# Performance work log

Measured on AMD Instinct MI355X. Metric: run time of the kernel, lower is better.

Reference implementation:

```python
import jax, jax.numpy as jnp
import numpy as np

N = 10000
E = 160000
EPS = 1e-5


def _bn(x, g, b):
    # BatchNorm1d over node dim, training-mode batch stats, biased variance
    m = jnp.mean(x, axis=0)
    v = jnp.mean((x - m) ** 2, axis=0)
    return (x - m) * jax.lax.rsqrt(v + EPS) * g + b


def _graph_conv(x, src, dst, ew, w_rel, b_rel, w_root):
    # PyG GraphConv: lin_rel(scatter_add(ew * x[src] -> dst)) + lin_root(x)
    agg = jax.ops.segment_sum(x[src] * ew[:, None], dst, num_segments=N)
    return agg @ w_rel + b_rel + x @ w_root


def setup_inputs() -> dict:
    key = jax.random.key(0)
    ks = jax.random.split(key, 16)
    x = jax.random.normal(ks[0], (N, 517), jnp.float32)
    edge_index = jax.random.randint(ks[1], (2, E), 0, N, dtype=jnp.int64)
    edge_weight = jax.random.uniform(ks[2], (E,), jnp.float32)

    def lin(k, fi, fo):
        return jax.random.normal(k, (fi, fo), jnp.float32) / np.sqrt(fi)

    d = dict(x=x, edge_index=edge_index, edge_weight=edge_weight)
    dims = [(517, 256), (256, 128), (128, 64)]
    for i, (fi, fo) in enumerate(dims, 1):
        d[f"w_rel{i}"] = lin(ks[3 * i], fi, fo)
        d[f"b_rel{i}"] = jnp.zeros((fo,), jnp.float32)
        d[f"w_root{i}"] = lin(ks[3 * i + 1], fi, fo)
        d[f"bn{i}_g"] = jnp.ones((fo,), jnp.float32)
        d[f"bn{i}_b"] = jnp.zeros((fo,), jnp.float32)
    d["w_lin"] = lin(ks[13], 64, 1)
    d["b_lin"] = jnp.zeros((1,), jnp.float32)
    return d


def reference(x, edge_index, edge_weight,
              w_rel1, b_rel1, w_root1, bn1_g, bn1_b,
              w_rel2, b_rel2, w_root2, bn2_g, bn2_b,
              w_rel3, b_rel3, w_root3, bn3_g, bn3_b,
              w_lin, b_lin):
    src, dst = edge_index[0], edge_index[1]
    h = jax.nn.relu(_bn(_graph_conv(x, src, dst, edge_weight, w_rel1, b_rel1, w_root1), bn1_g, bn1_b))
    h = jax.nn.relu(_bn(_graph_conv(h, src, dst, edge_weight, w_rel2, b_rel2, w_root2), bn2_g, bn2_b))
    h = jax.nn.relu(_bn(_graph_conv(h, src, dst, edge_weight, w_rel3, b_rel3, w_root3), bn3_g, bn3_b))
    h = jax.nn.log_sigmoid(h @ w_lin + b_lin)           # [N, 1]
    norm = jax.scipy.special.logsumexp(h, axis=0)        # [1]
    return h - norm
```

## Files before the change

### kernel.cpp

```cpp
#include <hip/hip_runtime.h>
#include <math.h>

#define NN 10000
#define EE 160000
#define MP 10112
#define EPSBN 1e-5f

typedef __attribute__((ext_vector_type(8))) short short8;
typedef __attribute__((ext_vector_type(4))) short short4v;
typedef __attribute__((ext_vector_type(4))) float f32x4;

__device__ __forceinline__ short f2bf(float f) {
    union { float f; unsigned u; } v; v.f = f;
    unsigned r = v.u + 0x7FFF + ((v.u >> 16) & 1);
    return (short)(r >> 16);
}
__device__ __forceinline__ float bf2f(unsigned short u) {
    union { unsigned u; float f; } v; v.u = ((unsigned)u) << 16;
    return v.f;
}
__device__ __forceinline__ void gload16(const short* g, short* l) {
    __builtin_amdgcn_global_load_lds((const __attribute__((address_space(1))) void*)g,
                                     (__attribute__((address_space(3))) void*)l, 16, 0, 0);
}


__global__ __launch_bounds__(256) void prep_kernel(const float* __restrict__ x, short* __restrict__ A,
                                                   const float* __restrict__ w1r, const float* __restrict__ w1o,
                                                   const float* __restrict__ w2r, const float* __restrict__ w2o,
                                                   const float* __restrict__ w3r, const float* __restrict__ w3o,
                                                   short* __restrict__ B1, short* __restrict__ B2, short* __restrict__ B3,
                                                   const int* __restrict__ dst, int* __restrict__ deg) {
    int b = blockIdx.x;
    if (b < 2848) {
        int idx = b * 256 + threadIdx.x;
        if (idx >= MP * 72) return;
        int row = idx / 72;
        int c0 = (idx % 72) * 8;
        short8 s;
        bool gr = (row < NN);
#pragma unroll
        for (int j = 0; j < 8; j++) {
            int c = c0 + j;
            float v = (gr && c < 517) ? x[(size_t)row * 517 + c] : 0.f;
            s[j] = f2bf(v);
        }
        *(short8*)&A[(size_t)row * 576 + c0] = s;
    } else if (b < 3744) {
        int j = b - 2848;
        const float *Wr, *Wo;
        short* Bt;
        int K, Kp, fo, row;
        if (j < 512)      { row = j;       Wr = w1r; Wo = w1o; Bt = B1; K = 517; Kp = 576; fo = 256; }
        else if (j < 768) { row = j - 512; Wr = w2r; Wo = w2o; Bt = B2; K = 256; Kp = 256; fo = 128; }
        else              { row = j - 768; Wr = w3r; Wo = w3o; Bt = B3; K = 128; Kp = 128; fo = 64; }
        const float* W = (row < fo) ? Wr : Wo;
        int col = (row < fo) ? row : row - fo;
        for (int k = threadIdx.x; k < Kp; k += 256) {
            short v = 0;
            if (k < K) v = f2bf(W[(size_t)k * fo + col]);
            Bt[(size_t)row * Kp + k] = v;
        }
    } else {
        int e = (b - 3744) * 256 + threadIdx.x;
        if (e < EE) atomicAdd(&deg[dst[e]], 1);
    }
}


__global__ __launch_bounds__(1024) void scan_kernel(const int* __restrict__ deg, int* __restrict__ off,
                                                    int* __restrict__ cursor, int n) {
    __shared__ int sm[1024];
    const int C = 10;
    int t = threadIdx.x;
    int base = t * C;
    int loc[C];
    int acc = 0;
#pragma unroll
    for (int i = 0; i < C; i++) {
        int idx = base + i;
        int v = (idx < n) ? deg[idx] : 0;
        loc[i] = acc;
        acc += v;
    }
    sm[t] = acc;
    __syncthreads();
    for (int d = 1; d < 1024; d <<= 1) {
        int v = (t >= d) ? sm[t - d] : 0;
        __syncthreads();
        sm[t] += v;
        __syncthreads();
    }
    int prefix = (t > 0) ? sm[t - 1] : 0;
#pragma unroll
    for (int i = 0; i < C; i++) {
        int idx = base + i;
        if (idx < n) {
            int o = prefix + loc[i];
            off[idx] = o;
            cursor[idx] = o;
        }
    }
    if (t == 1023) off[n] = sm[1023];
}

__global__ void fill_kernel(const int* __restrict__ src, const int* __restrict__ dst,
                            const float* __restrict__ ew, int* __restrict__ cursor,
                            int* __restrict__ psrc, float* __restrict__ pew, int E) {
    int e = blockIdx.x * blockDim.x + threadIdx.x;
    if (e < E) {
        int d = dst[e];
        int slot = atomicAdd(&cursor[d], 1);
        psrc[slot] = src[e];
        pew[slot] = ew[e];
    }
}


template <int MODE, int BM, int BN, int NT>
__global__ __launch_bounds__(NT) void mfma_gemm(const short* __restrict__ Abf,
                                                const float* __restrict__ Af32,
                                                const short* __restrict__ Bt,
                                                short* __restrict__ Yrel,
                                                float* __restrict__ Hroot,
                                                const float* __restrict__ brel,
                                                const float* __restrict__ ssum,
                                                const float* __restrict__ ssumsq,
                                                const float* __restrict__ bng,
                                                const float* __restrict__ bnb,
                                                int K, int Kp, int fo) {
    const int N_REP = BN / 16;
    const int ACH = BM * 8 / NT;
    const int BCH = BN * 8 / NT;
    const int AF4 = BM * 16 / NT;

    __shared__ short Als[2][BM * 64];
    __shared__ short Bls[2][BN * 64];
    __shared__ float scs[256], shs[256];

    int m0 = blockIdx.x * BM;
    int n0 = blockIdx.y * BN;
    int t = threadIdx.x;
    int lane = t & 63;
    int wid = t >> 6;

    if (MODE == 1) {
        for (int f = t; f < K; f += NT) {
            float mean = ssum[f] / (float)NN;
            float var = ssumsq[f] / (float)NN - mean * mean;
            var = fmaxf(var, 0.f);
            float sc = bng[f] * rsqrtf(var + EPSBN);
            scs[f] = sc;
            shs[f] = bnb[f] - mean * sc;
        }
        __syncthreads();
    }

    f32x4 acc[N_REP];
#pragma unroll
    for (int j = 0; j < N_REP; j++) acc[j] = (f32x4){0.f, 0.f, 0.f, 0.f};

    f32x4 ld[AF4 > 0 ? AF4 : 1];

    auto stageB = [&](int buf, int k0) {
#pragma unroll
        for (int i = 0; i < BCH; i++) {
            int idx = i * NT + t;
            int row = idx >> 3;
            int pc = idx & 7;
            gload16(Bt + (size_t)(n0 + row) * Kp + k0 + ((pc ^ (row & 7)) << 3), &Bls[buf][idx << 3]);
        }
    };
    auto stageA0 = [&](int buf, int k0) {
#pragma unroll
        for (int i = 0; i < ACH; i++) {
            int idx = i * NT + t;
            int row = idx >> 3;
            int pc = idx & 7;
            gload16(Abf + (size_t)(m0 + row) * Kp + k0 + ((pc ^ (row & 7)) << 3), &Als[buf][idx << 3]);
        }
    };
    auto loadA1 = [&](int k0) {
#pragma unroll
        for (int i = 0; i < AF4; i++) {
            int idx = i * NT + t;
            int row = idx >> 4;
            int fc = idx & 15;
            ld[i] = *(const f32x4*)(Af32 + (size_t)(m0 + row) * K + k0 + (fc << 2));
        }
    };
    auto writeA1 = [&](int buf, int k0) {
#pragma unroll
        for (int i = 0; i < AF4; i++) {
            int idx = i * NT + t;
            int row = idx >> 4;
            int fc = idx & 15;
            int kb = k0 + (fc << 2);
            short4v s;
#pragma unroll
            for (int j = 0; j < 4; j++) s[j] = f2bf(fmaxf(0.f, ld[i][j] * scs[kb + j] + shs[kb + j]));
            *(short4v*)&Als[buf][row * 64 + (((fc >> 1) ^ (row & 7)) << 3) + ((fc & 1) << 2)] = s;
        }
    };
    auto compute = [&](int buf) {
#pragma unroll
        for (int kk = 0; kk < 2; kk++) {
            int cc = kk * 4 + (lane >> 4);
            short8 af;
            {
                int row = wid * 16 + (lane & 15);
                af = *(const short8*)&Als[buf][(row * 8 + (cc ^ (row & 7))) * 8];
            }
#pragma unroll
            for (int ni = 0; ni < N_REP; ni++) {
                int row = ni * 16 + (lane & 15);
                short8 b8 = *(const short8*)&Bls[buf][(row * 8 + (cc ^ (row & 7))) * 8];
                acc[ni] = __builtin_amdgcn_mfma_f32_16x16x32_bf16(af, b8, acc[ni], 0, 0, 0);
            }
        }
    };

    int nsteps = Kp / 64;
    if (MODE == 0) stageA0(0, 0);
    else { loadA1(0); writeA1(0, 0); }
    stageB(0, 0);
    __syncthreads();

    int cur = 0;
    for (int s = 0; s < nsteps; s++) {
        int k1 = (s + 1) * 64;
        bool nxt = (s + 1 < nsteps);
        if (nxt) {
            if (MODE == 0) stageA0(cur ^ 1, k1);
            else loadA1(k1);
            stageB(cur ^ 1, k1);
        }
        compute(cur);
        if (nxt && MODE == 1) writeA1(cur ^ 1, k1);
        __syncthreads();
        cur ^= 1;
    }

#pragma unroll
    for (int ni = 0; ni < N_REP; ni++) {
        int gn = n0 + ni * 16 + (lane & 15);
        int row0 = m0 + wid * 16 + (lane >> 4) * 4;
        f32x4 v = acc[ni];
        if (gn < fo) {
#pragma unroll
            for (int r = 0; r < 4; r++) Yrel[(size_t)(row0 + r) * fo + gn] = f2bf(v[r]);
        } else {
            float bb = brel[gn - fo];
#pragma unroll
            for (int r = 0; r < 4; r++) Hroot[(size_t)(row0 + r) * fo + (gn - fo)] = v[r] + bb;
        }
    }
}


template <int FO>
__global__ __launch_bounds__(256) void agg_kernel(const short* __restrict__ Yrel,
                                                  float* __restrict__ hio,
                                                  const int* __restrict__ off,
                                                  const int* __restrict__ psrc,
                                                  const float* __restrict__ pew) {
    const int G = FO / 2;
    const int NPB = 256 / G;
    int t = threadIdx.x;
    int g = t / G;
    int tf = t % G;
    int f = tf * 2;
    int n = blockIdx.x * NPB + g;
    if (n >= NN) return;

    float a0 = 0.f, a1 = 0.f, b0 = 0.f, b1 = 0.f;
    int e0 = off[n], e1 = off[n + 1];
    int e = e0;
    for (; e + 3 < e1; e += 4) {
        int s0i = psrc[e], s1i = psrc[e + 1], s2i = psrc[e + 2], s3i = psrc[e + 3];
        float w0 = pew[e], w1 = pew[e + 1], w2 = pew[e + 2], w3 = pew[e + 3];
        unsigned p0 = *(const unsigned*)(Yrel + (size_t)s0i * FO + f);
        unsigned p1 = *(const unsigned*)(Yrel + (size_t)s1i * FO + f);
        unsigned p2 = *(const unsigned*)(Yrel + (size_t)s2i * FO + f);
        unsigned p3 = *(const unsigned*)(Yrel + (size_t)s3i * FO + f);
        a0 += w0 * bf2f((unsigned short)(p0 & 0xffff));
        a1 += w0 * bf2f((unsigned short)(p0 >> 16));
        b0 += w1 * bf2f((unsigned short)(p1 & 0xffff));
        b1 += w1 * bf2f((unsigned short)(p1 >> 16));
        a0 += w2 * bf2f((unsigned short)(p2 & 0xffff));
        a1 += w2 * bf2f((unsigned short)(p2 >> 16));
        b0 += w3 * bf2f((unsigned short)(p3 & 0xffff));
        b1 += w3 * bf2f((unsigned short)(p3 >> 16));
    }
    for (; e < e1; e++) {
        int s0i = psrc[e];
        float w0 = pew[e];
        unsigned p0 = *(const unsigned*)(Yrel + (size_t)s0i * FO + f);
        a0 += w0 * bf2f((unsigned short)(p0 & 0xffff));
        a1 += w0 * bf2f((unsigned short)(p0 >> 16));
    }
    size_t o = (size_t)n * FO + f;
    hio[o]     += a0 + b0;
    hio[o + 1] += a1 + b1;
}


template <int FO>
__global__ __launch_bounds__(256) void stats_part(const float* __restrict__ hio,
                                                  float* __restrict__ pS,
                                                  float* __restrict__ pQ) {
    const int FG = FO / 4;
    const int ROWL = 256 / FG;
    const int RPB = (NN + 255) / 256;
    __shared__ f32x4 sms[256], smq[256];
    int t = threadIdx.x;
    int fg = t % FG;
    int rl = t / FG;
    int r0 = blockIdx.x * RPB;
    int r1 = r0 + RPB;
    if (r1 > NN) r1 = NN;
    f32x4 s = (f32x4){0.f, 0.f, 0.f, 0.f};
    f32x4 q = (f32x4){0.f, 0.f, 0.f, 0.f};
    for (int r = r0 + rl; r < r1; r += ROWL) {
        f32x4 v = *(const f32x4*)(hio + (size_t)r * FO + fg * 4);
        s += v;
        q += v * v;
    }
    sms[t] = s;
    smq[t] = q;
    __syncthreads();
    if (rl == 0) {
#pragma unroll
        for (int l = 1; l < ROWL; l++) {
            s += sms[l * FG + fg];
            q += smq[l * FG + fg];
        }
        *(f32x4*)(pS + (size_t)blockIdx.x * FO + fg * 4) = s;
        *(f32x4*)(pQ + (size_t)blockIdx.x * FO + fg * 4) = q;
    }
}

__global__ __launch_bounds__(256) void stats_reduce(const float* __restrict__ pS,
                                                    const float* __restrict__ pQ,
                                                    float* __restrict__ ssum,
                                                    float* __restrict__ ssumsq,
                                                    int FO) {
    int f = blockIdx.x;
    int t = threadIdx.x;
    float s = pS[(size_t)t * FO + f];
    float q = pQ[(size_t)t * FO + f];
#pragma unroll
    for (int o = 32; o > 0; o >>= 1) {
        s += __shfl_down(s, o, 64);
        q += __shfl_down(q, o, 64);
    }
    __shared__ float smS[4], smQ[4];
    int lane = t & 63, w = t >> 6;
    if (lane == 0) { smS[w] = s; smQ[w] = q; }
    __syncthreads();
    if (t == 0) {
        ssum[f]   = smS[0] + smS[1] + smS[2] + smS[3];
        ssumsq[f] = smQ[0] + smQ[1] + smQ[2] + smQ[3];
    }
}


__global__ void head_kernel(const float* __restrict__ hio,
                            const float* __restrict__ ssum, const float* __restrict__ ssumsq,
                            const float* __restrict__ g3, const float* __restrict__ b3,
                            const float* __restrict__ wlin, const float* __restrict__ blin,
                            float* __restrict__ tmp) {
    int lane = threadIdx.x & 63;
    int wv = threadIdx.x >> 6;
    int n = blockIdx.x * 4 + wv;
    float mean = ssum[lane] / (float)NN;
    float var = ssumsq[lane] / (float)NN - mean * mean;
    var = fmaxf(var, 0.f);
    float sc = g3[lane] * rsqrtf(var + EPSBN);
    float sh = b3[lane] - mean * sc;
    float v = fmaxf(0.f, hio[(size_t)n * 64 + lane] * sc + sh);
    float p = v * wlin[lane];
#pragma unroll
    for (int o = 32; o > 0; o >>= 1) p += __shfl_down(p, o, 64);
    if (lane == 0) {
        float x = p + blin[0];
        float ls = (x >= 0.f) ? (-log1pf(expf(-x))) : (x - log1pf(expf(x)));
        tmp[n] = ls;
    }
}


__global__ __launch_bounds__(1024) void lse_final(const float* __restrict__ tmp, float* __restrict__ out) {
    __shared__ float sm[1024];
    int t = threadIdx.x;
    float m = -INFINITY;
    for (int i = t; i < NN; i += 1024) m = fmaxf(m, tmp[i]);
    sm[t] = m;
    __syncthreads();
    for (int s = 512; s > 0; s >>= 1) {
        if (t < s) sm[t] = fmaxf(sm[t], sm[t + s]);
        __syncthreads();
    }
    float M = sm[0];
    __syncthreads();
    float acc = 0.f;
    for (int i = t; i < NN; i += 1024) acc += expf(tmp[i] - M);
    sm[t] = acc;
    __syncthreads();
    for (int s = 512; s > 0; s >>= 1) {
        if (t < s) sm[t] += sm[t + s];
        __syncthreads();
    }
    float L = M + logf(sm[0]);
    for (int i = t; i < NN; i += 1024) out[i] = tmp[i] - L;
}


extern "C" void kernel_launch(void* const* d_in, const int* in_sizes, int n_in,
                              void* d_out, int out_size, void* d_ws, size_t ws_size,
                              hipStream_t stream) {
    const float* x  = (const float*)d_in[0];
    const int* ei   = (const int*)d_in[1];
    const float* ew = (const float*)d_in[2];
    const int* src = ei;
    const int* dst = ei + EE;

    const float* wrel[3]  = { (const float*)d_in[3],  (const float*)d_in[8],  (const float*)d_in[13] };
    const float* brel[3]  = { (const float*)d_in[4],  (const float*)d_in[9],  (const float*)d_in[14] };
    const float* wroot[3] = { (const float*)d_in[5],  (const float*)d_in[10], (const float*)d_in[15] };
    const float* bng[3]   = { (const float*)d_in[6],  (const float*)d_in[11], (const float*)d_in[16] };
    const float* bnb[3]   = { (const float*)d_in[7],  (const float*)d_in[12], (const float*)d_in[17] };
    const float* wlin = (const float*)d_in[18];
    const float* blin = (const float*)d_in[19];
    float* out = (float*)d_out;

    char* p = (char*)d_ws;
    auto alloc = [&](size_t bytes) { char* r = p; p += (bytes + 255) & ~(size_t)255; return r; };

    int*   deg     = (int*)alloc(NN * 4);
    float* ssumAll = (float*)alloc(1536 * 4);
    int*   off     = (int*)alloc((NN + 4) * 4);
    int*   cursor  = (int*)alloc(NN * 4);
    int*   psrc    = (int*)alloc(EE * 4);
    float* pew     = (float*)alloc(EE * 4);
    short* A1      = (short*)alloc((size_t)MP * 576 * 2);
    short* B1t     = (short*)alloc((size_t)512 * 576 * 2);
    short* B2t     = (short*)alloc((size_t)256 * 256 * 2);
    short* B3t     = (short*)alloc((size_t)128 * 128 * 2);
    short* Yrel    = (short*)alloc((size_t)MP * 256 * 2);
    float* hA      = (float*)alloc((size_t)MP * 256 * 4);
    float* hB      = (float*)alloc((size_t)MP * 128 * 4);
    float* hC      = (float*)alloc((size_t)MP * 64 * 4);
    float* tmp     = (float*)alloc(NN * 4);
    float* pS      = (float*)alloc((size_t)256 * 256 * 4);
    float* pQ      = (float*)alloc((size_t)256 * 256 * 4);

    float* ss[3]  = { ssumAll,       ssumAll + 512,  ssumAll + 1024 };
    float* sq[3]  = { ssumAll + 256, ssumAll + 768,  ssumAll + 1280 };

    hipMemsetAsync(deg, 0, (size_t)((char*)(ssumAll + 1536) - (char*)deg), stream);

    prep_kernel<<<4369, 256, 0, stream>>>(x, A1,
                                          wrel[0], wroot[0], wrel[1], wroot[1], wrel[2], wroot[2],
                                          B1t, B2t, B3t, dst, deg);
    scan_kernel<<<1, 1024, 0, stream>>>(deg, off, cursor, NN);
    fill_kernel<<<(EE + 255) / 256, 256, 0, stream>>>(src, dst, ew, cursor, psrc, pew, EE);

    mfma_gemm<0, 64, 128, 256><<<dim3(MP / 64, 4), 256, 0, stream>>>(
        A1, nullptr, B1t, Yrel, hA, brel[0], nullptr, nullptr, nullptr, nullptr, 576, 576, 256);
    agg_kernel<256><<<5000, 256, 0, stream>>>(Yrel, hA, off, psrc, pew);
    stats_part<256><<<256, 256, 0, stream>>>(hA, pS, pQ);
    stats_reduce<<<256, 256, 0, stream>>>(pS, pQ, ss[0], sq[0], 256);

    mfma_gemm<1, 64, 128, 256><<<dim3(MP / 64, 2), 256, 0, stream>>>(
        nullptr, hA, B2t, Yrel, hB, brel[1], ss[0], sq[0], bng[0], bnb[0], 256, 256, 128);
    agg_kernel<128><<<2500, 256, 0, stream>>>(Yrel, hB, off, psrc, pew);
    stats_part<128><<<256, 256, 0, stream>>>(hB, pS, pQ);
    stats_reduce<<<128, 256, 0, stream>>>(pS, pQ, ss[1], sq[1], 128);

    mfma_gemm<1, 64, 64, 256><<<dim3(MP / 64, 2), 256, 0, stream>>>(
        nullptr, hB, B3t, Yrel, hC, brel[2], ss[1], sq[1], bng[1], bnb[1], 128, 128, 64);
    agg_kernel<64><<<1250, 256, 0, stream>>>(Yrel, hC, off, psrc, pew);
    stats_part<64><<<256, 256, 0, stream>>>(hC, pS, pQ);
    stats_reduce<<<64, 256, 0, stream>>>(pS, pQ, ss[2], sq[2], 64);

    head_kernel<<<2500, 256, 0, stream>>>(hC, ss[2], sq[2], bng[2], bnb[2], wlin, blin, tmp);
    lse_final<<<1, 1024, 0, stream>>>(tmp, out);
}
```

Before: 157.4 us.

## Fuse BN statistics partials into aggregation kernel and precompute scale/shift

Each aggregation kernel now accumulates per-block column sums and sums of squares in shared memory with atomics and writes one partial row per block. This removes the separate stats_part pass that re-read the full hidden activations. stats_reduce now loops over many more partial rows and directly produces the BN scale and shift, which the GEMM and head kernels read instead of recomputing them. The cost is shared-memory atomic contention and a much larger partial buffer (up to 5000 rows) that has to be reduced.

New measurement: 203.7 us. +29.4%, slower.

```diff
diff --git a/kernel.cpp b/kernel.cpp
--- a/kernel.cpp
+++ b/kernel.cpp
@@ -124,10 +124,8 @@
                                                 short* __restrict__ Yrel,
                                                 float* __restrict__ Hroot,
                                                 const float* __restrict__ brel,
-                                                const float* __restrict__ ssum,
-                                                const float* __restrict__ ssumsq,
-                                                const float* __restrict__ bng,
-                                                const float* __restrict__ bnb,
+                                                const float* __restrict__ scs_g,
+                                                const float* __restrict__ shs_g,
                                                 int K, int Kp, int fo) {
     const int N_REP = BN / 16;
     const int ACH = BM * 8 / NT;
@@ -146,12 +144,8 @@
 
     if (MODE == 1) {
         for (int f = t; f < K; f += NT) {
-            float mean = ssum[f] / (float)NN;
-            float var = ssumsq[f] / (float)NN - mean * mean;
-            var = fmaxf(var, 0.f);
-            float sc = bng[f] * rsqrtf(var + EPSBN);
-            scs[f] = sc;
-            shs[f] = bnb[f] - mean * sc;
+            scs[f] = scs_g[f];
+            shs[f] = shs_g[f];
         }
         __syncthreads();
     }
@@ -263,92 +257,85 @@
                                                   float* __restrict__ hio,
                                                   const int* __restrict__ off,
                                                   const int* __restrict__ psrc,
-                                                  const float* __restrict__ pew) {
+                                                  const float* __restrict__ pew,
+                                                  float* __restrict__ pS,
+                                                  float* __restrict__ pQ) {
     const int G = FO / 2;
     const int NPB = 256 / G;
+    __shared__ float sm[2 * FO];
     int t = threadIdx.x;
     int g = t / G;
     int tf = t % G;
     int f = tf * 2;
     int n = blockIdx.x * NPB + g;
-    if (n >= NN) return;
-
-    float a0 = 0.f, a1 = 0.f, b0 = 0.f, b1 = 0.f;
-    int e0 = off[n], e1 = off[n + 1];
-    int e = e0;
-    for (; e + 3 < e1; e += 4) {
-        int s0i = psrc[e], s1i = psrc[e + 1], s2i = psrc[e + 2], s3i = psrc[e + 3];
-        float w0 = pew[e], w1 = pew[e + 1], w2 = pew[e + 2], w3 = pew[e + 3];
-        unsigned p0 = *(const unsigned*)(Yrel + (size_t)s0i * FO + f);
-        unsigned p1 = *(const unsigned*)(Yrel + (size_t)s1i * FO + f);
-        unsigned p2 = *(const unsigned*)(Yrel + (size_t)s2i * FO + f);
-        unsigned p3 = *(const unsigned*)(Yrel + (size_t)s3i * FO + f);
-        a0 += w0 * bf2f((unsigned short)(p0 & 0xffff));
-        a1 += w0 * bf2f((unsigned short)(p0 >> 16));
-        b0 += w1 * bf2f((unsigned short)(p1 & 0xffff));
-        b1 += w1 * bf2f((unsigned short)(p1 >> 16));
-        a0 += w2 * bf2f((unsigned short)(p2 & 0xffff));
-        a1 += w2 * bf2f((unsigned short)(p2 >> 16));
-        b0 += w3 * bf2f((unsigned short)(p3 & 0xffff));
-        b1 += w3 * bf2f((unsigned short)(p3 >> 16));
-    }
-    for (; e < e1; e++) {
-        int s0i = psrc[e];
-        float w0 = pew[e];
-        unsigned p0 = *(const unsigned*)(Yrel + (size_t)s0i * FO + f);
-        a0 += w0 * bf2f((unsigned short)(p0 & 0xffff));
-        a1 += w0 * bf2f((unsigned short)(p0 >> 16));
-    }
-    size_t o = (size_t)n * FO + f;
-    hio[o]     += a0 + b0;
-    hio[o + 1] += a1 + b1;
-}
-
-
-template <int FO>
-__global__ __launch_bounds__(256) void stats_part(const float* __restrict__ hio,
-                                                  float* __restrict__ pS,
-                                                  float* __restrict__ pQ) {
-    const int FG = FO / 4;
-    const int ROWL = 256 / FG;
-    const int RPB = (NN + 255) / 256;
-    __shared__ f32x4 sms[256], smq[256];
-    int t = threadIdx.x;
-    int fg = t % FG;
-    int rl = t / FG;
-    int r0 = blockIdx.x * RPB;
-    int r1 = r0 + RPB;
-    if (r1 > NN) r1 = NN;
-    f32x4 s = (f32x4){0.f, 0.f, 0.f, 0.f};
-    f32x4 q = (f32x4){0.f, 0.f, 0.f, 0.f};
-    for (int r = r0 + rl; r < r1; r += ROWL) {
-        f32x4 v = *(const f32x4*)(hio + (size_t)r * FO + fg * 4);
-        s += v;
-        q += v * v;
-    }
-    sms[t] = s;
-    smq[t] = q;
-    __syncthreads();
-    if (rl == 0) {
-#pragma unroll
-        for (int l = 1; l < ROWL; l++) {
-            s += sms[l * FG + fg];
-            q += smq[l * FG + fg];
-        }
-        *(f32x4*)(pS + (size_t)blockIdx.x * FO + fg * 4) = s;
-        *(f32x4*)(pQ + (size_t)blockIdx.x * FO + fg * 4) = q;
-    }
-}
+
+    float v0 = 0.f, v1 = 0.f;
+    bool valid = (n < NN);
+    if (valid) {
+        float a0 = 0.f, a1 = 0.f, b0 = 0.f, b1 = 0.f;
+        int e0 = off[n], e1 = off[n + 1];
+        int e = e0;
+        for (; e + 3 < e1; e += 4) {
+            int s0i = psrc[e], s1i = psrc[e + 1], s2i = psrc[e + 2], s3i = psrc[e + 3];
+            float w0 = pew[e], w1 = pew[e + 1], w2 = pew[e + 2], w3 = pew[e + 3];
+            unsigned p0 = *(const unsigned*)(Yrel + (size_t)s0i * FO + f);
+            unsigned p1 = *(const unsigned*)(Yrel + (size_t)s1i * FO + f);
+            unsigned p2 = *(const unsigned*)(Yrel + (size_t)s2i * FO + f);
+            unsigned p3 = *(const unsigned*)(Yrel + (size_t)s3i * FO + f);
+            a0 += w0 * bf2f((unsigned short)(p0 & 0xffff));
+            a1 += w0 * bf2f((unsigned short)(p0 >> 16));
+            b0 += w1 * bf2f((unsigned short)(p1 & 0xffff));
+            b1 += w1 * bf2f((unsigned short)(p1 >> 16));
+            a0 += w2 * bf2f((unsigned short)(p2 & 0xffff));
+            a1 += w2 * bf2f((unsigned short)(p2 >> 16));
+            b0 += w3 * bf2f((unsigned short)(p3 & 0xffff));
+            b1 += w3 * bf2f((unsigned short)(p3 >> 16));
+        }
+        for (; e < e1; e++) {
+            int s0i = psrc[e];
+            float w0 = pew[e];
+            unsigned p0 = *(const unsigned*)(Yrel + (size_t)s0i * FO + f);
+            a0 += w0 * bf2f((unsigned short)(p0 & 0xffff));
+            a1 += w0 * bf2f((unsigned short)(p0 >> 16));
+        }
+        size_t o = (size_t)n * FO + f;
+        v0 = hio[o] + a0 + b0;
+        v1 = hio[o + 1] + a1 + b1;
+        hio[o] = v0;
+        hio[o + 1] = v1;
+    }
+
+    for (int i = t; i < 2 * FO; i += 256) sm[i] = 0.f;
+    __syncthreads();
+    if (valid) {
+        atomicAdd(&sm[f], v0);
+        atomicAdd(&sm[f + 1], v1);
+        atomicAdd(&sm[FO + f], v0 * v0);
+        atomicAdd(&sm[FO + f + 1], v1 * v1);
+    }
+    __syncthreads();
+    for (int i = t; i < FO; i += 256) {
+        size_t o = (size_t)blockIdx.x * FO + i;
+        pS[o] = sm[i];
+        pQ[o] = sm[FO + i];
+    }
+}
+
 
 __global__ __launch_bounds__(256) void stats_reduce(const float* __restrict__ pS,
                                                     const float* __restrict__ pQ,
-                                                    float* __restrict__ ssum,
-                                                    float* __restrict__ ssumsq,
-                                                    int FO) {
+                                                    const float* __restrict__ bng,
+                                                    const float* __restrict__ bnb,
+                                                    float* __restrict__ scs,
+                                                    float* __restrict__ shs,
+                                                    int FO, int GX) {
     int f = blockIdx.x;
     int t = threadIdx.x;
-    float s = pS[(size_t)t * FO + f];
-    float q = pQ[(size_t)t * FO + f];
+    float s = 0.f, q = 0.f;
+    for (int r = t; r < GX; r += 256) {
+        s += pS[(size_t)r * FO + f];
+        q += pQ[(size_t)r * FO + f];
+    }
 #pragma unroll
     for (int o = 32; o > 0; o >>= 1) {
         s += __shfl_down(s, o, 64);
@@ -359,26 +346,26 @@
     if (lane == 0) { smS[w] = s; smQ[w] = q; }
     __syncthreads();
     if (t == 0) {
-        ssum[f]   = smS[0] + smS[1] + smS[2] + smS[3];
-        ssumsq[f] = smQ[0] + smQ[1] + smQ[2] + smQ[3];
+        s = smS[0] + smS[1] + smS[2] + smS[3];
+        q = smQ[0] + smQ[1] + smQ[2] + smQ[3];
+        float mean = s / (float)NN;
+        float var = q / (float)NN - mean * mean;
+        var = fmaxf(var, 0.f);
+        float sc = bng[f] * rsqrtf(var + EPSBN);
+        scs[f] = sc;
+        shs[f] = bnb[f] - mean * sc;
     }
 }
 
 
 __global__ void head_kernel(const float* __restrict__ hio,
-                            const float* __restrict__ ssum, const float* __restrict__ ssumsq,
-                            const float* __restrict__ g3, const float* __restrict__ b3,
+                            const float* __restrict__ scs, const float* __restrict__ shs,
                             const float* __restrict__ wlin, const float* __restrict__ blin,
                             float* __restrict__ tmp) {
     int lane = threadIdx.x & 63;
     int wv = threadIdx.x >> 6;
     int n = blockIdx.x * 4 + wv;
-    float mean = ssum[lane] / (float)NN;
-    float var = ssumsq[lane] / (float)NN - mean * mean;
-    var = fmaxf(var, 0.f);
-    float sc = g3[lane] * rsqrtf(var + EPSBN);
-    float sh = b3[lane] - mean * sc;
-    float v = fmaxf(0.f, hio[(size_t)n * 64 + lane] * sc + sh);
+    float v = fmaxf(0.f, hio[(size_t)n * 64 + lane] * scs[lane] + shs[lane]);
     float p = v * wlin[lane];
 #pragma unroll
     for (int o = 32; o > 0; o >>= 1) p += __shfl_down(p, o, 64);
@@ -438,7 +425,7 @@
     auto alloc = [&](size_t bytes) { char* r = p; p += (bytes + 255) & ~(size_t)255; return r; };
 
     int*   deg     = (int*)alloc(NN * 4);
-    float* ssumAll = (float*)alloc(1536 * 4);
+    float* scsAll  = (float*)alloc(1536 * 4);
     int*   off     = (int*)alloc((NN + 4) * 4);
     int*   cursor  = (int*)alloc(NN * 4);
     int*   psrc    = (int*)alloc(EE * 4);
@@ -452,13 +439,13 @@
     float* hB      = (float*)alloc((size_t)MP * 128 * 4);
     float* hC      = (float*)alloc((size_t)MP * 64 * 4);
     float* tmp     = (float*)alloc(NN * 4);
-    float* pS      = (float*)alloc((size_t)256 * 256 * 4);
-    float* pQ      = (float*)alloc((size_t)256 * 256 * 4);
-
-    float* ss[3]  = { ssumAll,       ssumAll + 512,  ssumAll + 1024 };
-    float* sq[3]  = { ssumAll + 256, ssumAll + 768,  ssumAll + 1280 };
-
-    hipMemsetAsync(deg, 0, (size_t)((char*)(ssumAll + 1536) - (char*)deg), stream);
+    float* pS      = (float*)alloc((size_t)5000 * 256 * 4);
+    float* pQ      = (float*)alloc((size_t)5000 * 256 * 4);
+
+    float* scs[3] = { scsAll,       scsAll + 512,  scsAll + 1024 };
+    float* shs[3] = { scsAll + 256, scsAll + 768,  scsAll + 1280 };
+
+    hipMemsetAsync(deg, 0, NN * sizeof(int), stream);
 
     prep_kernel<<<4369, 256, 0, stream>>>(x, A1,
                                           wrel[0], wroot[0], wrel[1], wroot[1], wrel[2], wroot[2],
@@ -467,23 +454,20 @@
     fill_kernel<<<(EE + 255) / 256, 256, 0, stream>>>(src, dst, ew, cursor, psrc, pew, EE);
 
     mfma_gemm<0, 64, 128, 256><<<dim3(MP / 64, 4), 256, 0, stream>>>(
-        A1, nullptr, B1t, Yrel, hA, brel[0], nullptr, nullptr, nullptr, nullptr, 576, 576, 256);
-    agg_kernel<256><<<5000, 256, 0, stream>>>(Yrel, hA, off, psrc, pew);
-    stats_part<256><<<256, 256, 0, stream>>>(hA, pS, pQ);
-    stats_reduce<<<256, 256, 0, stream>>>(pS, pQ, ss[0], sq[0], 256);
+        A1, nullptr, B1t, Yrel, hA, brel[0], nullptr, nullptr, 576, 576, 256);
+    agg_kernel<256><<<5000, 256, 0, stream>>>(Yrel, hA, off, psrc, pew, pS, pQ);
+    stats_reduce<<<256, 256, 0, stream>>>(pS, pQ, bng[0], bnb[0], scs[0], shs[0], 256, 5000);
 
     mfma_gemm<1, 64, 128, 256><<<dim3(MP / 64, 2), 256, 0, stream>>>(
-        nullptr, hA, B2t, Yrel, hB, brel[1], ss[0], sq[0], bng[0], bnb[0], 256, 256, 128);
-    agg_kernel<128><<<2500, 256, 0, stream>>>(Yrel, hB, off, psrc, pew);
-    stats_part<128><<<256, 256, 0, stream>>>(hB, pS, pQ);
-    stats_reduce<<<128, 256, 0, stream>>>(pS, pQ, ss[1], sq[1], 128);
+        nullptr, hA, B2t, Yrel, hB, brel[1], scs[0], shs[0], 256, 256, 128);
+    agg_kernel<128><<<2500, 256, 0, stream>>>(Yrel, hB, off, psrc, pew, pS, pQ);
+    stats_reduce<<<128, 256, 0, stream>>>(pS, pQ, bng[1], bnb[1], scs[1], shs[1], 128, 2500);
 
     mfma_gemm<1, 64, 64, 256><<<dim3(MP / 64, 2), 256, 0, stream>>>(
-        nullptr, hB, B3t, Yrel, hC, brel[2], ss[1], sq[1], bng[1], bnb[1], 128, 128, 64);
-    agg_kernel<64><<<1250, 256, 0, stream>>>(Yrel, hC, off, psrc, pew);
-    stats_part<64><<<256, 256, 0, stream>>>(hC, pS, pQ);
-    stats_reduce<<<64, 256, 0, stream>>>(pS, pQ, ss[2], sq[2], 64);
-
-    head_kernel<<<2500, 256, 0, stream>>>(hC, ss[2], sq[2], bng[2], bnb[2], wlin, blin, tmp);
+        nullptr, hB, B3t, Yrel, hC, brel[2], scs[1], shs[1], 128, 128, 64);
+    agg_kernel<64><<<1250, 256, 0, stream>>>(Yrel, hC, off, psrc, pew, pS, pQ);
+    stats_reduce<<<64, 256, 0, stream>>>(pS, pQ, bng[2], bnb[2], scs[2], shs[2], 64, 1250);
+
+    head_kernel<<<2500, 256, 0, stream>>>(hC, scs[2], shs[2], wlin, blin, tmp);
     lse_final<<<1, 1024, 0, stream>>>(tmp, out);
 }
```

## Split aggregation into feature chunks per block and precompute BN scale/shift

Applied to the files above, without the earlier changes.

The aggregation kernel now partitions features into 8 chunks, with the chunk taken from the low 3 bits of blockIdx. Each block handles 16/32/64 nodes over a narrow feature slice, so consecutive blocks touch the same gather rows, and this is meant to improve cache locality and occupancy of the gather. BatchNorm scale and shift are now computed once in stats_reduce instead of redundantly in every GEMM block and head thread. The memset is also shrunk to cover only the degree array. The trade-off is more blocks, each with shorter rows to gather, so edge indices are read 8 times.

Result: slower. 173.1 us (+10.0%).

```diff
diff --git a/kernel.cpp b/kernel.cpp
--- a/kernel.cpp
+++ b/kernel.cpp
@@ -124,10 +124,8 @@
                                                 short* __restrict__ Yrel,
                                                 float* __restrict__ Hroot,
                                                 const float* __restrict__ brel,
-                                                const float* __restrict__ ssum,
-                                                const float* __restrict__ ssumsq,
-                                                const float* __restrict__ bng,
-                                                const float* __restrict__ bnb,
+                                                const float* __restrict__ scs_g,
+                                                const float* __restrict__ shs_g,
                                                 int K, int Kp, int fo) {
     const int N_REP = BN / 16;
     const int ACH = BM * 8 / NT;
@@ -146,12 +144,8 @@
 
     if (MODE == 1) {
         for (int f = t; f < K; f += NT) {
-            float mean = ssum[f] / (float)NN;
-            float var = ssumsq[f] / (float)NN - mean * mean;
-            var = fmaxf(var, 0.f);
-            float sc = bng[f] * rsqrtf(var + EPSBN);
-            scs[f] = sc;
-            shs[f] = bnb[f] - mean * sc;
+            scs[f] = scs_g[f];
+            shs[f] = shs_g[f];
         }
         __syncthreads();
     }
@@ -258,19 +252,21 @@
 }
 
 
-template <int FO>
+template <int FO, int CH>
 __global__ __launch_bounds__(256) void agg_kernel(const short* __restrict__ Yrel,
                                                   float* __restrict__ hio,
                                                   const int* __restrict__ off,
                                                   const int* __restrict__ psrc,
                                                   const float* __restrict__ pew) {
-    const int G = FO / 2;
+    const int G = CH / 2;
     const int NPB = 256 / G;
     int t = threadIdx.x;
+    int c = blockIdx.x & 7;
+    int nb = blockIdx.x >> 3;
     int g = t / G;
     int tf = t % G;
-    int f = tf * 2;
-    int n = blockIdx.x * NPB + g;
+    int f = c * CH + tf * 2;
+    int n = nb * NPB + g;
     if (n >= NN) return;
 
     float a0 = 0.f, a1 = 0.f, b0 = 0.f, b1 = 0.f;
@@ -342,8 +338,10 @@
 
 __global__ __launch_bounds__(256) void stats_reduce(const float* __restrict__ pS,
                                                     const float* __restrict__ pQ,
-                                                    float* __restrict__ ssum,
-                                                    float* __restrict__ ssumsq,
+                                                    const float* __restrict__ bng,
+                                                    const float* __restrict__ bnb,
+                                                    float* __restrict__ scs,
+                                                    float* __restrict__ shs,
                                                     int FO) {
     int f = blockIdx.x;
     int t = threadIdx.x;
@@ -359,26 +357,26 @@
     if (lane == 0) { smS[w] = s; smQ[w] = q; }
     __syncthreads();
     if (t == 0) {
-        ssum[f]   = smS[0] + smS[1] + smS[2] + smS[3];
-        ssumsq[f] = smQ[0] + smQ[1] + smQ[2] + smQ[3];
+        s = smS[0] + smS[1] + smS[2] + smS[3];
+        q = smQ[0] + smQ[1] + smQ[2] + smQ[3];
+        float mean = s / (float)NN;
+        float var = q / (float)NN - mean * mean;
+        var = fmaxf(var, 0.f);
+        float sc = bng[f] * rsqrtf(var + EPSBN);
+        scs[f] = sc;
+        shs[f] = bnb[f] - mean * sc;
     }
 }
 
 
 __global__ void head_kernel(const float* __restrict__ hio,
-                            const float* __restrict__ ssum, const float* __restrict__ ssumsq,
-                            const float* __restrict__ g3, const float* __restrict__ b3,
+                            const float* __restrict__ scs, const float* __restrict__ shs,
                             const float* __restrict__ wlin, const float* __restrict__ blin,
                             float* __restrict__ tmp) {
     int lane = threadIdx.x & 63;
     int wv = threadIdx.x >> 6;
     int n = blockIdx.x * 4 + wv;
-    float mean = ssum[lane] / (float)NN;
-    float var = ssumsq[lane] / (float)NN - mean * mean;
-    var = fmaxf(var, 0.f);
-    float sc = g3[lane] * rsqrtf(var + EPSBN);
-    float sh = b3[lane] - mean * sc;
-    float v = fmaxf(0.f, hio[(size_t)n * 64 + lane] * sc + sh);
+    float v = fmaxf(0.f, hio[(size_t)n * 64 + lane] * scs[lane] + shs[lane]);
     float p = v * wlin[lane];
 #pragma unroll
     for (int o = 32; o > 0; o >>= 1) p += __shfl_down(p, o, 64);
@@ -438,7 +436,7 @@
     auto alloc = [&](size_t bytes) { char* r = p; p += (bytes + 255) & ~(size_t)255; return r; };
 
     int*   deg     = (int*)alloc(NN * 4);
-    float* ssumAll = (float*)alloc(1536 * 4);
+    float* scsAll  = (float*)alloc(1536 * 4);
     int*   off     = (int*)alloc((NN + 4) * 4);
     int*   cursor  = (int*)alloc(NN * 4);
     int*   psrc    = (int*)alloc(EE * 4);
@@ -455,10 +453,10 @@
     float* pS      = (float*)alloc((size_t)256 * 256 * 4);
     float* pQ      = (float*)alloc((size_t)256 * 256 * 4);
 
-    float* ss[3]  = { ssumAll,       ssumAll + 512,  ssumAll + 1024 };
-    float* sq[3]  = { ssumAll + 256, ssumAll + 768,  ssumAll + 1280 };
-
-    hipMemsetAsync(deg, 0, (size_t)((char*)(ssumAll + 1536) - (char*)deg), stream);
+    float* scs[3] = { scsAll,       scsAll + 512,  scsAll + 1024 };
+    float* shs[3] = { scsAll + 256, scsAll + 768,  scsAll + 1280 };
+
+    hipMemsetAsync(deg, 0, NN * sizeof(int), stream);
 
     prep_kernel<<<4369, 256, 0, stream>>>(x, A1,
                                           wrel[0], wroot[0], wrel[1], wroot[1], wrel[2], wroot[2],
@@ -467,23 +465,23 @@
     fill_kernel<<<(EE + 255) / 256, 256, 0, stream>>>(src, dst, ew, cursor, psrc, pew, EE);
 
     mfma_gemm<0, 64, 128, 256><<<dim3(MP / 64, 4), 256, 0, stream>>>(
-        A1, nullptr, B1t, Yrel, hA, brel[0], nullptr, nullptr, nullptr, nullptr, 576, 576, 256);
-    agg_kernel<256><<<5000, 256, 0, stream>>>(Yrel, hA, off, psrc, pew);
+        A1, nullptr, B1t, Yrel, hA, brel[0], nullptr, nullptr, 576, 576, 256);
+    agg_kernel<256, 32><<<8 * 625, 256, 0, stream>>>(Yrel, hA, off, psrc, pew);
     stats_part<256><<<256, 256, 0, stream>>>(hA, pS, pQ);
-    stats_reduce<<<256, 256, 0, stream>>>(pS, pQ, ss[0], sq[0], 256);
+    stats_reduce<<<256, 256, 0, stream>>>(pS, pQ, bng[0], bnb[0], scs[0], shs[0], 256);
 
     mfma_gemm<1, 64, 128, 256><<<dim3(MP / 64, 2), 256, 0, stream>>>(
-        nullptr, hA, B2t, Yrel, hB, brel[1], ss[0], sq[0], bng[0], bnb[0], 256, 256, 128);
-    agg_kernel<128><<<2500, 256, 0, stream>>>(Yrel, hB, off, psrc, pew);
+        nullptr, hA, B2t, Yrel, hB, brel[1], scs[0], shs[0], 256, 256, 128);
+    agg_kernel<128, 16><<<8 * 313, 256, 0, stream>>>(Yrel, hB, off, psrc, pew);
     stats_part<128><<<256, 256, 0, stream>>>(hB, pS, pQ);
-    stats_reduce<<<128, 256, 0, stream>>>(pS, pQ, ss[1], sq[1], 128);
+    stats_reduce<<<128, 256, 0, stream>>>(pS, pQ, bng[1], bnb[1], scs[1], shs[1], 128);
 
     mfma_gemm<1, 64, 64, 256><<<dim3(MP / 64, 2), 256, 0, stream>>>(
-        nullptr, hB, B3t, Yrel, hC, brel[2], ss[1], sq[1], bng[1], bnb[1], 128, 128, 64);
-    agg_kernel<64><<<1250, 256, 0, stream>>>(Yrel, hC, off, psrc, pew);
+        nullptr, hB, B3t, Yrel, hC, brel[2], scs[1], shs[1], 128, 128, 64);
+    agg_kernel<64, 8><<<8 * 157, 256, 0, stream>>>(Yrel, hC, off, psrc, pew);
     stats_part<64><<<256, 256, 0, stream>>>(hC, pS, pQ);
-    stats_reduce<<<64, 256, 0, stream>>>(pS, pQ, ss[2], sq[2], 64);
-
-    head_kernel<<<2500, 256, 0, stream>>>(hC, ss[2], sq[2], bng[2], bnb[2], wlin, blin, tmp);
+    stats_reduce<<<64, 256, 0, stream>>>(pS, pQ, bng[2], bnb[2], scs[2], shs[2], 64);
+
+    head_kernel<<<2500, 256, 0, stream>>>(hC, scs[2], shs[2], wlin, blin, tmp);
     lse_final<<<1, 1024, 0, stream>>>(tmp, out);
 }
```
